# Kernel tuning notes

Hardware: AMD Instinct MI355X
Metric: run time of the kernel (lower is better)

Reference implementation:

```python
import jax, jax.numpy as jnp
import numpy as np

BIG = 1e8   # fill value used by to_dense_batch for missing neighbors in the original
EPS_W = 1e-8
EPS_BN = 1e-5


def setup_inputs() -> dict:
    key = jax.random.key(0)
    ks = jax.random.split(key, 8)
    N, S, Dc, Df = 16384, 4096, 256, 64
    fine_xyz = jax.random.normal(ks[0], (1, 3, N), dtype=jnp.float32)
    coarse_xyz = jax.random.normal(ks[1], (1, 3, S), dtype=jnp.float32)
    fine_piece_id = jnp.sort(jax.random.randint(ks[2], (1, 1, N), 0, 4))
    coarse_piece_id = jnp.sort(jax.random.randint(ks[3], (1, 1, S), 0, 4))
    fine_features = jax.random.normal(ks[4], (1, Df, N), dtype=jnp.float32)
    coarse_features = jax.random.normal(ks[5], (1, Dc, S), dtype=jnp.float32)
    # mlp stack: Conv1d(320->256), Conv1d(256->128), each with BatchNorm1d
    W1 = jax.random.normal(ks[6], (256, Dc + Df), dtype=jnp.float32) * 0.05
    b1 = jnp.zeros((256,), jnp.float32)
    g1 = jnp.ones((256,), jnp.float32)
    be1 = jnp.zeros((256,), jnp.float32)
    W2 = jax.random.normal(ks[7], (128, 256), dtype=jnp.float32) * 0.05
    b2 = jnp.zeros((128,), jnp.float32)
    g2 = jnp.ones((128,), jnp.float32)
    be2 = jnp.zeros((128,), jnp.float32)
    return dict(fine_xyz=fine_xyz, coarse_xyz=coarse_xyz,
                fine_piece_id=fine_piece_id, coarse_piece_id=coarse_piece_id,
                fine_features=fine_features, coarse_features=coarse_features,
                W1=W1, b1=b1, g1=g1, be1=be1, W2=W2, b2=b2, g2=g2, be2=be2)


def _bn_relu(x, gamma, beta):
    # x: [N, C]; BatchNorm1d in training mode -> batch stats over the N axis
    mu = jnp.mean(x, axis=0, keepdims=True)
    var = jnp.mean((x - mu) ** 2, axis=0, keepdims=True)  # biased var, as torch BN
    return jax.nn.relu((x - mu) * jax.lax.rsqrt(var + EPS_BN) * gamma + beta)


def reference(fine_xyz, coarse_xyz, fine_piece_id, coarse_piece_id,
              fine_features, coarse_features, W1, b1, g1, be1, W2, b2, g2, be2):
    fxyz = fine_xyz[0].T            # [N, 3]
    cxyz = coarse_xyz[0].T          # [S, 3]
    ff = fine_features[0].T         # [N, Df]
    cf = coarse_features[0].T       # [S, Dc]
    fid = fine_piece_id.reshape(-1)     # [N]
    cid = coarse_piece_id.reshape(-1)   # [S]

    # squared euclidean distances, masked to the same piece (knn with batch vectors)
    d2 = (jnp.sum(fxyz ** 2, -1)[:, None] + jnp.sum(cxyz ** 2, -1)[None, :]
          - 2.0 * fxyz @ cxyz.T)                       # [N, S]
    d2 = jnp.where(fid[:, None] != cid[None, :], BIG, d2)

    neg_d, idx = jax.lax.top_k(-d2, 3)                  # 3-NN per fine point
    dist = -neg_d                                       # [N, 3]

    w = 1.0 / (dist + EPS_W)
    w = w / jnp.sum(w, axis=1, keepdims=True)           # [N, 3]

    gathered = cf[idx]                                  # [N, 3, Dc]
    interp = jnp.sum(gathered * w[:, :, None], axis=1)  # [N, Dc]

    x = jnp.concatenate([interp, ff], axis=-1)          # [N, Dc+Df]
    x = _bn_relu(x @ W1.T + b1, g1, be1)                # [N, 256]
    x = _bn_relu(x @ W2.T + b2, g2, be2)                # [N, 128]
    return x.T[None]                                    # [1, 128, N]
```

## Files before the change

kernel.cpp:

```cpp
#include <hip/hip_runtime.h>
#include <hip/hip_bf16.h>

#define N_FINE   16384
#define S_COARSE 4096
#define DC       256
#define DF       64
#define K1       320
#define C1       256
#define C2       128
#define BIGF     1e8f
#define EPS_W    1e-8f
#define EPS_BN   1e-5f

typedef __attribute__((ext_vector_type(8))) short bf16x8;
typedef __attribute__((ext_vector_type(8))) unsigned short u16x8;
typedef __attribute__((ext_vector_type(4))) float f32x4;

#define OFF_RANGES 0
#define OFF_SUMS   256
#define OFF_SCALE1 3328
#define OFF_SHIFT1 4352
#define OFF_SCALE2 5376
#define OFF_SHIFT2 5888
#define OFF_CPACK  8192
#define OFF_CFT    73728
#define OFF_IDX3   4268032
#define OFF_W3     4464640
#define OFF_W1B    4661248
#define OFF_W2B    4825088
#define OFF_Y1     4890624
#define OFF_Y2     13279232

__device__ inline unsigned short f2bf_bits(float f) {
    __hip_bfloat16 h = __float2bfloat16(f);
    unsigned short u;
    __builtin_memcpy(&u, &h, 2);
    return u;
}

__global__ __launch_bounds__(256) void setup_kernel(
    const int* __restrict__ cid, int* __restrict__ ranges, float* __restrict__ sums,
    const float* __restrict__ cxyz, float4* __restrict__ cpack,
    const float* __restrict__ W1, const float* __restrict__ W2,
    unsigned short* __restrict__ W1b, unsigned short* __restrict__ W2b,
    const float* __restrict__ cf, float* __restrict__ cfT)
{
    __shared__ float tile[32][33];
    int b = blockIdx.x, t = threadIdx.x;
    if (b == 0) {
        if (t < 8) ranges[t] = 0;
        for (int i = t; i < 768; i += 256) sums[i] = 0.f;
        __syncthreads();
        for (int s = t; s < S_COARSE; s += 256) {
            int c = cid[s];
            if (s == 0 || cid[s - 1] != c) ranges[c] = s;
            if (s == S_COARSE - 1 || cid[s + 1] != c) ranges[4 + c] = s + 1;
        }
    } else if (b <= 16) {
        int s = (b - 1) * 256 + t;
        float x = cxyz[s], y = cxyz[S_COARSE + s], z = cxyz[2 * S_COARSE + s];
        cpack[s] = make_float4(x, y, z, x * x + y * y + z * z);
    } else if (b <= 336) {
        int i = (b - 17) * 256 + t;
        W1b[i] = f2bf_bits(W1[i]);
        if (i < C2 * C1) W2b[i] = f2bf_bits(W2[i]);
    } else {
        int lb = b - 337;
        int tx = t & 31, ty = t >> 5;
        int s0 = (lb & 127) * 32, c0 = (lb >> 7) * 32;
        #pragma unroll
        for (int i = 0; i < 4; i++)
            tile[ty + i * 8][tx] = cf[(c0 + ty + i * 8) * S_COARSE + s0 + tx];
        __syncthreads();
        #pragma unroll
        for (int i = 0; i < 4; i++) {
            int s = ty + i * 8;
            cfT[(s0 + s) * DC + c0 + tx] = tile[tx][s];
        }
    }
}

__global__ __launch_bounds__(256) void knn_kernel(const float* __restrict__ fxyz,
                                                  const int* __restrict__ fpid,
                                                  const float4* __restrict__ cpack,
                                                  const int* __restrict__ ranges,
                                                  int* __restrict__ idx3,
                                                  float* __restrict__ w3) {
    __shared__ float md[16][16][3];
    __shared__ int   mi[16][16][3];
    int t = threadIdx.x;
    int p = t & 15, ch = t >> 4;
    int n = blockIdx.x * 16 + p;
    int fid = fpid[n];
    float fx = fxyz[n], fy = fxyz[N_FINE + n], fz = fxyz[2 * N_FINE + n];
    float fn2 = fx * fx + fy * fy + fz * fz;
    int st = ranges[fid], en = ranges[4 + fid];
    int cnt = en - st;
    int L = (cnt + 15) >> 4;
    int cs = st + ch * L;
    int ce = min(cs + L, en);
    float d0 = BIGF, d1 = BIGF, d2v = BIGF;
    int i0 = -1, i1 = -1, i2 = -1;
    for (int s = cs; s < ce; ++s) {
        float4 c = cpack[s];
        float d = fn2 + c.w - 2.0f * (fx * c.x + fy * c.y + fz * c.z);
        if (d < d0)       { d2v = d1; i2 = i1; d1 = d0; i1 = i0; d0 = d; i0 = s; }
        else if (d < d1)  { d2v = d1; i2 = i1; d1 = d;  i1 = s; }
        else if (d < d2v) { d2v = d;  i2 = s; }
    }
    md[p][ch][0] = d0;  md[p][ch][1] = d1;  md[p][ch][2] = d2v;
    mi[p][ch][0] = i0;  mi[p][ch][1] = i1;  mi[p][ch][2] = i2;
    __syncthreads();
    if (t < 16) {
        d0 = d1 = d2v = BIGF; i0 = i1 = i2 = -1;
        for (int c = 0; c < 16; c++) {
            #pragma unroll
            for (int k = 0; k < 3; k++) {
                int ii = mi[t][c][k];
                if (ii < 0) continue;
                float d = md[t][c][k];
                if (d < d0)       { d2v = d1; i2 = i1; d1 = d0; i1 = i0; d0 = d; i0 = ii; }
                else if (d < d1)  { d2v = d1; i2 = i1; d1 = d;  i1 = ii; }
                else if (d < d2v) { d2v = d;  i2 = ii; }
            }
        }
        int cand = 0;
        while (i0 < 0 || i1 < 0 || i2 < 0) {
            if (cand >= st && cand < en) { cand = en; continue; }
            if (i0 < 0)      { i0 = cand; d0 = BIGF; }
            else if (i1 < 0) { i1 = cand; d1 = BIGF; }
            else             { i2 = cand; d2v = BIGF; }
            cand++;
        }
        float w0 = 1.0f / (d0 + EPS_W);
        float w1 = 1.0f / (d1 + EPS_W);
        float w2 = 1.0f / (d2v + EPS_W);
        float inv = 1.0f / (w0 + w1 + w2);
        idx3[n * 3 + 0] = i0; idx3[n * 3 + 1] = i1; idx3[n * 3 + 2] = i2;
        w3[n * 3 + 0] = w0 * inv; w3[n * 3 + 1] = w1 * inv; w3[n * 3 + 2] = w2 * inv;
    }
}

__global__ __launch_bounds__(256) void gemm1_kernel(
    const int* __restrict__ idx3, const float* __restrict__ w3,
    const float* __restrict__ cfT, const float* __restrict__ ff,
    const unsigned short* __restrict__ W1b, const float* __restrict__ bias,
    unsigned short* __restrict__ Y1, float* __restrict__ sums, float* __restrict__ sumsq)
{
    __shared__ __align__(16) unsigned short As[4 * 32 * 8];
    __shared__ __align__(16) unsigned short Bs[4 * 256 * 8];
    __shared__ int   sI[32][3];
    __shared__ float sWt[32][3];
    int t = threadIdx.x;
    int m0 = blockIdx.x * 32;
    int lane = t & 63, wid = t >> 6;
    int wn = wid * 64;

    if (t < 32) {
        sI[t][0]  = idx3[(m0 + t) * 3 + 0];
        sI[t][1]  = idx3[(m0 + t) * 3 + 1];
        sI[t][2]  = idx3[(m0 + t) * 3 + 2];
        sWt[t][0] = w3[(m0 + t) * 3 + 0];
        sWt[t][1] = w3[(m0 + t) * 3 + 1];
        sWt[t][2] = w3[(m0 + t) * 3 + 2];
    }
    int ksA = t & 3, rowA = t >> 2;
    int fxw = ksA << 2;
    int gA = ksA * 32 + (rowA ^ fxw);
    int rowB = t;
    f32x4 acc[2][4] = {};
    int ks = lane >> 4, r16 = lane & 15, fxr = ks << 2;
    __syncthreads();

    for (int kt = 0; kt < K1; kt += 32) {
        u16x8 va;
        if (t < 128) {
            int k0 = kt + ksA * 8;
            if (k0 < DC) {
                int i0 = sI[rowA][0], i1 = sI[rowA][1], i2 = sI[rowA][2];
                float w0 = sWt[rowA][0], w1 = sWt[rowA][1], w2 = sWt[rowA][2];
                const float* c0p = &cfT[i0 * DC + k0];
                const float* c1p = &cfT[i1 * DC + k0];
                const float* c2p = &cfT[i2 * DC + k0];
                float4 a0 = *(const float4*)c0p, a1 = *(const float4*)(c0p + 4);
                float4 b0 = *(const float4*)c1p, b1 = *(const float4*)(c1p + 4);
                float4 e0 = *(const float4*)c2p, e1 = *(const float4*)(c2p + 4);
                va[0] = f2bf_bits(w0 * a0.x + w1 * b0.x + w2 * e0.x);
                va[1] = f2bf_bits(w0 * a0.y + w1 * b0.y + w2 * e0.y);
                va[2] = f2bf_bits(w0 * a0.z + w1 * b0.z + w2 * e0.z);
                va[3] = f2bf_bits(w0 * a0.w + w1 * b0.w + w2 * e0.w);
                va[4] = f2bf_bits(w0 * a1.x + w1 * b1.x + w2 * e1.x);
                va[5] = f2bf_bits(w0 * a1.y + w1 * b1.y + w2 * e1.y);
                va[6] = f2bf_bits(w0 * a1.z + w1 * b1.z + w2 * e1.z);
                va[7] = f2bf_bits(w0 * a1.w + w1 * b1.w + w2 * e1.w);
            } else {
                int c = k0 - DC;
                #pragma unroll
                for (int i = 0; i < 8; i++)
                    va[i] = f2bf_bits(ff[(c + i) * N_FINE + m0 + rowA]);
            }
        }
        u16x8 vb[4];
        #pragma unroll
        for (int kb = 0; kb < 4; kb++)
            vb[kb] = *(const u16x8*)&W1b[(size_t)rowB * K1 + kt + kb * 8];
        __syncthreads();
        if (t < 128) *(u16x8*)&As[gA * 8] = va;
        #pragma unroll
        for (int kb = 0; kb < 4; kb++)
            *(u16x8*)&Bs[(kb * 256 + (rowB ^ (kb << 2))) * 8] = vb[kb];
        __syncthreads();
        bf16x8 af[2], bfr[4];
        #pragma unroll
        for (int mi = 0; mi < 2; mi++)
            af[mi] = *(const bf16x8*)&As[(ks * 32 + ((mi * 16 + r16) ^ fxr)) * 8];
        #pragma unroll
        for (int nj = 0; nj < 4; nj++)
            bfr[nj] = *(const bf16x8*)&Bs[(ks * 256 + ((wn + nj * 16 + r16) ^ fxr)) * 8];
        #pragma unroll
        for (int mi = 0; mi < 2; mi++)
            #pragma unroll
            for (int nj = 0; nj < 4; nj++)
                acc[mi][nj] = __builtin_amdgcn_mfma_f32_16x16x32_bf16(af[mi], bfr[nj], acc[mi][nj], 0, 0, 0);
    }

    float sl[4] = {0.f, 0.f, 0.f, 0.f}, s2l[4] = {0.f, 0.f, 0.f, 0.f};
    #pragma unroll
    for (int nj = 0; nj < 4; nj++) {
        int n = wn + nj * 16 + r16;
        float bb = bias[n];
        #pragma unroll
        for (int mi = 0; mi < 2; mi++) {
            #pragma unroll
            for (int r = 0; r < 4; r++) {
                int m = m0 + mi * 16 + ks * 4 + r;
                float o = acc[mi][nj][r] + bb;
                Y1[(size_t)m * C1 + n] = f2bf_bits(o);
                sl[nj] += o; s2l[nj] += o * o;
            }
        }
    }
    #pragma unroll
    for (int nj = 0; nj < 4; nj++) {
        sl[nj]  += __shfl_xor(sl[nj],  16, 64);
        sl[nj]  += __shfl_xor(sl[nj],  32, 64);
        s2l[nj] += __shfl_xor(s2l[nj], 16, 64);
        s2l[nj] += __shfl_xor(s2l[nj], 32, 64);
    }
    if (lane < 16) {
        #pragma unroll
        for (int nj = 0; nj < 4; nj++) {
            atomicAdd(&sums[wn + nj * 16 + lane],  sl[nj]);
            atomicAdd(&sumsq[wn + nj * 16 + lane], s2l[nj]);
        }
    }
}

template <int KDIM, int NOUT>
__global__ __launch_bounds__(256) void mfma_gemm2_kernel(
    const unsigned short* __restrict__ A,
    const unsigned short* __restrict__ B,
    const float* __restrict__ bias,
    const float* __restrict__ scale,
    const float* __restrict__ shift,
    float* __restrict__ Yout,
    float* __restrict__ sums, float* __restrict__ sumsq)
{
    __shared__ __align__(16) unsigned short As[4 * 128 * 8];
    __shared__ __align__(16) unsigned short Bs[4 * 64 * 8];
    int t = threadIdx.x;
    int m0 = blockIdx.x * 128, j0 = blockIdx.y * 64;
    int lane = t & 63, wid = t >> 6;
    int wm = (wid >> 1) * 64, wn = (wid & 1) * 32;

    int ksA = t & 3;
    int rowA0 = t >> 2;
    int rowA1 = 64 + rowA0;
    int fxw = ksA << 2;
    int gA0 = ksA * 128 + (rowA0 ^ fxw);
    int gA1 = ksA * 128 + (rowA1 ^ fxw);
    int gB  = ksA * 64 + (rowA0 ^ fxw);
    const unsigned short* pa0 = A + (size_t)(m0 + rowA0) * KDIM + ksA * 8;
    const unsigned short* pa1 = A + (size_t)(m0 + rowA1) * KDIM + ksA * 8;
    const unsigned short* pb  = B + (size_t)(j0 + rowA0) * KDIM + ksA * 8;

    f32x4 acc[4][2] = {};
    int ks = lane >> 4, r16 = lane & 15;
    int fxr = ks << 2;

    for (int kt = 0; kt < KDIM; kt += 32) {
        u16x8 va0 = *(const u16x8*)(pa0 + kt);
        u16x8 va1 = *(const u16x8*)(pa1 + kt);
        u16x8 vb  = *(const u16x8*)(pb + kt);
        int kb = kt + ksA * 8;
        #pragma unroll
        for (int i = 0; i < 8; i++) {
            float sc = scale[kb + i], sh = shift[kb + i];
            float f0 = __uint_as_float(((unsigned)va0[i]) << 16);
            float f1 = __uint_as_float(((unsigned)va1[i]) << 16);
            va0[i] = f2bf_bits(fmaxf(fmaf(f0, sc, sh), 0.f));
            va1[i] = f2bf_bits(fmaxf(fmaf(f1, sc, sh), 0.f));
        }
        __syncthreads();
        *(u16x8*)&As[gA0 * 8] = va0;
        *(u16x8*)&As[gA1 * 8] = va1;
        *(u16x8*)&Bs[gB * 8]  = vb;
        __syncthreads();
        bf16x8 af[4], bfr[2];
        #pragma unroll
        for (int mi = 0; mi < 4; mi++)
            af[mi] = *(const bf16x8*)&As[(ks * 128 + wm + mi * 16 + (r16 ^ fxr)) * 8];
        #pragma unroll
        for (int nj = 0; nj < 2; nj++)
            bfr[nj] = *(const bf16x8*)&Bs[(ks * 64 + wn + nj * 16 + (r16 ^ fxr)) * 8];
        #pragma unroll
        for (int mi = 0; mi < 4; mi++)
            #pragma unroll
            for (int nj = 0; nj < 2; nj++)
                acc[mi][nj] = __builtin_amdgcn_mfma_f32_16x16x32_bf16(af[mi], bfr[nj], acc[mi][nj], 0, 0, 0);
    }

    float sl[2] = {0.f, 0.f}, s2l[2] = {0.f, 0.f};
    #pragma unroll
    for (int nj = 0; nj < 2; nj++) {
        int n = j0 + wn + nj * 16 + r16;
        float bb = bias[n];
        #pragma unroll
        for (int mi = 0; mi < 4; mi++) {
            #pragma unroll
            for (int r = 0; r < 4; r++) {
                int m = m0 + wm + mi * 16 + ks * 4 + r;
                float o = acc[mi][nj][r] + bb;
                Yout[(size_t)m * NOUT + n] = o;
                sl[nj] += o; s2l[nj] += o * o;
            }
        }
    }
    #pragma unroll
    for (int nj = 0; nj < 2; nj++) {
        sl[nj]  += __shfl_xor(sl[nj],  16, 64);
        sl[nj]  += __shfl_xor(sl[nj],  32, 64);
        s2l[nj] += __shfl_xor(s2l[nj], 16, 64);
        s2l[nj] += __shfl_xor(s2l[nj], 32, 64);
    }
    if (lane < 16) {
        atomicAdd(&sums[j0 + wn + lane],       sl[0]);
        atomicAdd(&sums[j0 + wn + 16 + lane],  sl[1]);
        atomicAdd(&sumsq[j0 + wn + lane],      s2l[0]);
        atomicAdd(&sumsq[j0 + wn + 16 + lane], s2l[1]);
    }
}

__global__ void finalize_kernel(const float* __restrict__ sums, const float* __restrict__ sumsq,
                                const float* __restrict__ g, const float* __restrict__ be,
                                float* __restrict__ scale, float* __restrict__ shift, int C) {
    int t = threadIdx.x;
    if (t < C) {
        float mean = sums[t] * (1.0f / N_FINE);
        float var = sumsq[t] * (1.0f / N_FINE) - mean * mean;
        float sc = g[t] * rsqrtf(var + EPS_BN);
        scale[t] = sc;
        shift[t] = be[t] - mean * sc;
    }
}

__global__ __launch_bounds__(256) void out_kernel(const float* __restrict__ Y2,
                                                  const float* __restrict__ scale2,
                                                  const float* __restrict__ shift2,
                                                  float* __restrict__ out) {
    __shared__ float tile[64][65];
    int t = threadIdx.x;
    int n0 = blockIdx.x * 64, c0 = blockIdx.y * 64;
    int cl = t & 63, rg = t >> 6;
    #pragma unroll
    for (int i = 0; i < 16; i++) {
        int r = rg + i * 4;
        tile[r][cl] = Y2[(n0 + r) * C2 + c0 + cl];
    }
    __syncthreads();
    #pragma unroll
    for (int i = 0; i < 16; i++) {
        int c = rg + i * 4;
        float v = fmaf(tile[cl][c], scale2[c0 + c], shift2[c0 + c]);
        out[(c0 + c) * N_FINE + n0 + cl] = fmaxf(v, 0.f);
    }
}

extern "C" void kernel_launch(void* const* d_in, const int* in_sizes, int n_in,
                              void* d_out, int out_size, void* d_ws, size_t ws_size,
                              hipStream_t stream) {
    const float* fine_xyz   = (const float*)d_in[0];
    const float* coarse_xyz = (const float*)d_in[1];
    const int*   fine_pid   = (const int*)d_in[2];
    const int*   coarse_pid = (const int*)d_in[3];
    const float* fine_feat  = (const float*)d_in[4];
    const float* coarse_feat= (const float*)d_in[5];
    const float* W1  = (const float*)d_in[6];
    const float* b1  = (const float*)d_in[7];
    const float* g1  = (const float*)d_in[8];
    const float* be1 = (const float*)d_in[9];
    const float* W2  = (const float*)d_in[10];
    const float* b2  = (const float*)d_in[11];
    const float* g2  = (const float*)d_in[12];
    const float* be2 = (const float*)d_in[13];
    float* out = (float*)d_out;

    char* ws = (char*)d_ws;
    int*    ranges = (int*)(ws + OFF_RANGES);
    float*  sums1  = (float*)(ws + OFF_SUMS);
    float*  sumsq1 = sums1 + 256;
    float*  sums2  = sums1 + 512;
    float*  sumsq2 = sums1 + 640;
    float*  scale1 = (float*)(ws + OFF_SCALE1);
    float*  shift1 = (float*)(ws + OFF_SHIFT1);
    float*  scale2 = (float*)(ws + OFF_SCALE2);
    float*  shift2 = (float*)(ws + OFF_SHIFT2);
    float4* cpack  = (float4*)(ws + OFF_CPACK);
    float*  cfT    = (float*)(ws + OFF_CFT);
    int*    idx3   = (int*)(ws + OFF_IDX3);
    float*  w3     = (float*)(ws + OFF_W3);
    unsigned short* W1b = (unsigned short*)(ws + OFF_W1B);
    unsigned short* W2b = (unsigned short*)(ws + OFF_W2B);
    unsigned short* Y1  = (unsigned short*)(ws + OFF_Y1);
    float*          Y2  = (float*)(ws + OFF_Y2);

    setup_kernel<<<1361, 256, 0, stream>>>(coarse_pid, ranges, sums1,
                                           coarse_xyz, cpack, W1, W2, W1b, W2b,
                                           coarse_feat, cfT);
    knn_kernel<<<N_FINE / 16, 256, 0, stream>>>(fine_xyz, fine_pid, cpack, ranges, idx3, w3);

    gemm1_kernel<<<N_FINE / 32, 256, 0, stream>>>(idx3, w3, cfT, fine_feat,
                                                  W1b, b1, Y1, sums1, sumsq1);
    finalize_kernel<<<1, 256, 0, stream>>>(sums1, sumsq1, g1, be1, scale1, shift1, C1);

    mfma_gemm2_kernel<C1, C2><<<dim3(N_FINE / 128, C2 / 64), 256, 0, stream>>>(
        Y1, W2b, b2, scale1, shift1, Y2, sums2, sumsq2);
    finalize_kernel<<<1, 256, 0, stream>>>(sums2, sumsq2, g2, be2, scale2, shift2, C2);

    out_kernel<<<dim3(N_FINE / 64, C2 / 64), 256, 0, stream>>>(Y2, scale2, shift2, out);
}
```

Baseline: 182.7 us.

## Use one wavefront per fine point in kNN and fuse BN finalize into GEMMs

```diff
diff --git a/kernel.cpp b/kernel.cpp
--- a/kernel.cpp
+++ b/kernel.cpp
@@ -11,11 +11,13 @@
 #define BIGF     1e8f
 #define EPS_W    1e-8f
 #define EPS_BN   1e-5f
+#define IMAX     0x7fffffff
 
 typedef __attribute__((ext_vector_type(8))) short bf16x8;
 typedef __attribute__((ext_vector_type(8))) unsigned short u16x8;
 typedef __attribute__((ext_vector_type(4))) float f32x4;
 
+#define OFF_CNT    128
 #define OFF_RANGES 0
 #define OFF_SUMS   256
 #define OFF_SCALE1 3328
@@ -40,6 +42,7 @@
 
 __global__ __launch_bounds__(256) void setup_kernel(
     const int* __restrict__ cid, int* __restrict__ ranges, float* __restrict__ sums,
+    int* __restrict__ cnt,
     const float* __restrict__ cxyz, float4* __restrict__ cpack,
     const float* __restrict__ W1, const float* __restrict__ W2,
     unsigned short* __restrict__ W1b, unsigned short* __restrict__ W2b,
@@ -49,6 +52,7 @@
     int b = blockIdx.x, t = threadIdx.x;
     if (b == 0) {
         if (t < 8) ranges[t] = 0;
+        if (t < 2) cnt[t] = 0;
         for (int i = t; i < 768; i += 256) sums[i] = 0.f;
         __syncthreads();
         for (int s = t; s < S_COARSE; s += 256) {
@@ -86,50 +90,46 @@
                                                   const int* __restrict__ ranges,
                                                   int* __restrict__ idx3,
                                                   float* __restrict__ w3) {
-    __shared__ float md[16][16][3];
-    __shared__ int   mi[16][16][3];
     int t = threadIdx.x;
-    int p = t & 15, ch = t >> 4;
-    int n = blockIdx.x * 16 + p;
+    int lane = t & 63, wid = t >> 6;
+    int n = blockIdx.x * 4 + wid;
     int fid = fpid[n];
     float fx = fxyz[n], fy = fxyz[N_FINE + n], fz = fxyz[2 * N_FINE + n];
     float fn2 = fx * fx + fy * fy + fz * fz;
     int st = ranges[fid], en = ranges[4 + fid];
-    int cnt = en - st;
-    int L = (cnt + 15) >> 4;
-    int cs = st + ch * L;
-    int ce = min(cs + L, en);
+
     float d0 = BIGF, d1 = BIGF, d2v = BIGF;
-    int i0 = -1, i1 = -1, i2 = -1;
-    for (int s = cs; s < ce; ++s) {
+    int i0 = IMAX, i1 = IMAX, i2 = IMAX;
+    for (int s = st + lane; s < en; s += 64) {
         float4 c = cpack[s];
         float d = fn2 + c.w - 2.0f * (fx * c.x + fy * c.y + fz * c.z);
         if (d < d0)       { d2v = d1; i2 = i1; d1 = d0; i1 = i0; d0 = d; i0 = s; }
         else if (d < d1)  { d2v = d1; i2 = i1; d1 = d;  i1 = s; }
         else if (d < d2v) { d2v = d;  i2 = s; }
     }
-    md[p][ch][0] = d0;  md[p][ch][1] = d1;  md[p][ch][2] = d2v;
-    mi[p][ch][0] = i0;  mi[p][ch][1] = i1;  mi[p][ch][2] = i2;
-    __syncthreads();
-    if (t < 16) {
-        d0 = d1 = d2v = BIGF; i0 = i1 = i2 = -1;
-        for (int c = 0; c < 16; c++) {
-            #pragma unroll
-            for (int k = 0; k < 3; k++) {
-                int ii = mi[t][c][k];
-                if (ii < 0) continue;
-                float d = md[t][c][k];
-                if (d < d0)       { d2v = d1; i2 = i1; d1 = d0; i1 = i0; d0 = d; i0 = ii; }
-                else if (d < d1)  { d2v = d1; i2 = i1; d1 = d;  i1 = ii; }
-                else if (d < d2v) { d2v = d;  i2 = ii; }
-            }
-        }
+    #pragma unroll
+    for (int m = 1; m < 64; m <<= 1) {
+        float e0 = __shfl_xor(d0, m, 64), e1 = __shfl_xor(d1, m, 64), e2 = __shfl_xor(d2v, m, 64);
+        int   j0 = __shfl_xor(i0, m, 64), j1 = __shfl_xor(i1, m, 64), j2 = __shfl_xor(i2, m, 64);
+        #pragma unroll
+        for (int q = 0; q < 3; q++) {
+            float e = (q == 0) ? e0 : (q == 1) ? e1 : e2;
+            int   j = (q == 0) ? j0 : (q == 1) ? j1 : j2;
+            bool b0 = (e < d0) || (e == d0 && j < i0);
+            bool b1 = (e < d1) || (e == d1 && j < i1);
+            bool b2 = (e < d2v) || (e == d2v && j < i2);
+            if (b0)      { d2v = d1; i2 = i1; d1 = d0; i1 = i0; d0 = e; i0 = j; }
+            else if (b1) { d2v = d1; i2 = i1; d1 = e;  i1 = j; }
+            else if (b2) { d2v = e;  i2 = j; }
+        }
+    }
+    if (lane == 0) {
         int cand = 0;
-        while (i0 < 0 || i1 < 0 || i2 < 0) {
+        while (i0 == IMAX || i1 == IMAX || i2 == IMAX) {
             if (cand >= st && cand < en) { cand = en; continue; }
-            if (i0 < 0)      { i0 = cand; d0 = BIGF; }
-            else if (i1 < 0) { i1 = cand; d1 = BIGF; }
-            else             { i2 = cand; d2v = BIGF; }
+            if (i0 == IMAX)      { i0 = cand; d0 = BIGF; }
+            else if (i1 == IMAX) { i1 = cand; d1 = BIGF; }
+            else                 { i2 = cand; d2v = BIGF; }
             cand++;
         }
         float w0 = 1.0f / (d0 + EPS_W);
@@ -145,12 +145,15 @@
     const int* __restrict__ idx3, const float* __restrict__ w3,
     const float* __restrict__ cfT, const float* __restrict__ ff,
     const unsigned short* __restrict__ W1b, const float* __restrict__ bias,
-    unsigned short* __restrict__ Y1, float* __restrict__ sums, float* __restrict__ sumsq)
+    unsigned short* __restrict__ Y1, float* __restrict__ sums, float* __restrict__ sumsq,
+    const float* __restrict__ g, const float* __restrict__ be,
+    float* __restrict__ scale, float* __restrict__ shift, int* __restrict__ cnt)
 {
     __shared__ __align__(16) unsigned short As[4 * 32 * 8];
     __shared__ __align__(16) unsigned short Bs[4 * 256 * 8];
     __shared__ int   sI[32][3];
     __shared__ float sWt[32][3];
+    __shared__ int isLast;
     int t = threadIdx.x;
     int m0 = blockIdx.x * 32;
     int lane = t & 63, wid = t >> 6;
@@ -254,6 +257,19 @@
             atomicAdd(&sumsq[wn + nj * 16 + lane], s2l[nj]);
         }
     }
+    __threadfence();
+    __syncthreads();
+    if (t == 0) isLast = (atomicAdd(cnt, 1) == (int)gridDim.x - 1);
+    __syncthreads();
+    if (isLast && t < C1) {
+        float s  = atomicAdd(&sums[t], 0.f);
+        float s2 = atomicAdd(&sumsq[t], 0.f);
+        float mean = s * (1.0f / N_FINE);
+        float var = s2 * (1.0f / N_FINE) - mean * mean;
+        float sc = g[t] * rsqrtf(var + EPS_BN);
+        scale[t] = sc;
+        shift[t] = be[t] - mean * sc;
+    }
 }
 
 template <int KDIM, int NOUT>
@@ -264,10 +280,13 @@
     const float* __restrict__ scale,
     const float* __restrict__ shift,
     float* __restrict__ Yout,
-    float* __restrict__ sums, float* __restrict__ sumsq)
+    float* __restrict__ sums, float* __restrict__ sumsq,
+    const float* __restrict__ g, const float* __restrict__ be,
+    float* __restrict__ scale2, float* __restrict__ shift2, int* __restrict__ cnt)
 {
     __shared__ __align__(16) unsigned short As[4 * 128 * 8];
     __shared__ __align__(16) unsigned short Bs[4 * 64 * 8];
+    __shared__ int isLast;
     int t = threadIdx.x;
     int m0 = blockIdx.x * 128, j0 = blockIdx.y * 64;
     int lane = t & 63, wid = t >> 6;
@@ -349,18 +368,18 @@
         atomicAdd(&sumsq[j0 + wn + lane],      s2l[0]);
         atomicAdd(&sumsq[j0 + wn + 16 + lane], s2l[1]);
     }
-}
-
-__global__ void finalize_kernel(const float* __restrict__ sums, const float* __restrict__ sumsq,
-                                const float* __restrict__ g, const float* __restrict__ be,
-                                float* __restrict__ scale, float* __restrict__ shift, int C) {
-    int t = threadIdx.x;
-    if (t < C) {
-        float mean = sums[t] * (1.0f / N_FINE);
-        float var = sumsq[t] * (1.0f / N_FINE) - mean * mean;
+    __threadfence();
+    __syncthreads();
+    if (t == 0) isLast = (atomicAdd(cnt, 1) == (int)(gridDim.x * gridDim.y) - 1);
+    __syncthreads();
+    if (isLast && t < NOUT) {
+        float s  = atomicAdd(&sums[t], 0.f);
+        float s2 = atomicAdd(&sumsq[t], 0.f);
+        float mean = s * (1.0f / N_FINE);
+        float var = s2 * (1.0f / N_FINE) - mean * mean;
         float sc = g[t] * rsqrtf(var + EPS_BN);
-        scale[t] = sc;
-        shift[t] = be[t] - mean * sc;
+        scale2[t] = sc;
+        shift2[t] = be[t] - mean * sc;
     }
 }
 
@@ -407,6 +426,7 @@
 
     char* ws = (char*)d_ws;
     int*    ranges = (int*)(ws + OFF_RANGES);
+    int*    cnt    = (int*)(ws + OFF_CNT);
     float*  sums1  = (float*)(ws + OFF_SUMS);
     float*  sumsq1 = sums1 + 256;
     float*  sums2  = sums1 + 512;
@@ -424,18 +444,18 @@
     unsigned short* Y1  = (unsigned short*)(ws + OFF_Y1);
     float*          Y2  = (float*)(ws + OFF_Y2);
 
-    setup_kernel<<<1361, 256, 0, stream>>>(coarse_pid, ranges, sums1,
+    setup_kernel<<<1361, 256, 0, stream>>>(coarse_pid, ranges, sums1, cnt,
                                            coarse_xyz, cpack, W1, W2, W1b, W2b,
                                            coarse_feat, cfT);
-    knn_kernel<<<N_FINE / 16, 256, 0, stream>>>(fine_xyz, fine_pid, cpack, ranges, idx3, w3);
+    knn_kernel<<<N_FINE / 4, 256, 0, stream>>>(fine_xyz, fine_pid, cpack, ranges, idx3, w3);
 
     gemm1_kernel<<<N_FINE / 32, 256, 0, stream>>>(idx3, w3, cfT, fine_feat,
-                                                  W1b, b1, Y1, sums1, sumsq1);
-    finalize_kernel<<<1, 256, 0, stream>>>(sums1, sumsq1, g1, be1, scale1, shift1, C1);
+                                                  W1b, b1, Y1, sums1, sumsq1,
+                                                  g1, be1, scale1, shift1, cnt);
 
     mfma_gemm2_kernel<C1, C2><<<dim3(N_FINE / 128, C2 / 64), 256, 0, stream>>>(
-        Y1, W2b, b2, scale1, shift1, Y2, sums2, sumsq2);
-    finalize_kernel<<<1, 256, 0, stream>>>(sums2, sumsq2, g2, be2, scale2, shift2, C2);
+        Y1, W2b, b2, scale1, shift1, Y2, sums2, sumsq2,
+        g2, be2, scale2, shift2, cnt + 1);
 
     out_kernel<<<dim3(N_FINE / 64, C2 / 64), 256, 0, stream>>>(Y2, scale2, shift2, out);
 }
```

After: 224.3 us. 1.23x slower.
